# Kernel optimization log

Hardware: AMD Instinct MI355X
Metric: run time of the kernel (lower is better)

The kernel has to match this reference:

```python
import jax, jax.numpy as jnp
import numpy as np

N = 50000
E = 1000000
NODE_IN = 1281
H = 256
L = 4
NUM_RADIAL = 16
CUTOFF = 10.0
PROJ = 128
NUM_CLASSES = 4
MSG_IN = H + 3 + NUM_RADIAL  # 275


def layer_norm(x, g, b, eps=1e-5):
    m = jnp.mean(x, axis=-1, keepdims=True)
    v = jnp.var(x, axis=-1, keepdims=True)
    return (x - m) * jax.lax.rsqrt(v + eps) * g + b


def setup_inputs() -> dict:
    key = jax.random.key(0)
    ks = jax.random.split(key, 32)
    inp = {}
    inp['x'] = jax.random.normal(ks[0], (N, NODE_IN), dtype=jnp.float32)
    inp['pos'] = jax.random.normal(ks[1], (N, 3), dtype=jnp.float32) * 5.0
    inp['edge_index'] = jax.random.randint(ks[2], (2, E), 0, N, dtype=jnp.int32)
    s = lambda k, shp, fan: jax.random.normal(k, shp, dtype=jnp.float32) * (1.0 / np.sqrt(fan))
    # node encoder: Linear(1281->256), SiLU, Linear(256->256), LayerNorm
    inp['ne_W1'] = s(ks[3], (NODE_IN, H), NODE_IN); inp['ne_b1'] = jnp.zeros((H,), jnp.float32)
    inp['ne_W2'] = s(ks[4], (H, H), H); inp['ne_b2'] = jnp.zeros((H,), jnp.float32)
    inp['ne_g'] = jnp.ones((H,), jnp.float32); inp['ne_beta'] = jnp.zeros((H,), jnp.float32)
    # conv layers (stacked over L): Linear(275->256) + LayerNorm, plus outer LayerNorms
    inp['convW'] = s(ks[5], (L, MSG_IN, H), MSG_IN)
    inp['convB'] = jnp.zeros((L, H), jnp.float32)
    inp['convG'] = jnp.ones((L, H), jnp.float32); inp['convBeta'] = jnp.zeros((L, H), jnp.float32)
    inp['lnG'] = jnp.ones((L, H), jnp.float32); inp['lnB'] = jnp.zeros((L, H), jnp.float32)
    # attention pool gate: Linear(256->64), SiLU, Linear(64->1)
    inp['pgW1'] = s(ks[6], (H, H // 4), H); inp['pgb1'] = jnp.zeros((H // 4,), jnp.float32)
    inp['pgW2'] = s(ks[7], (H // 4, 1), H // 4); inp['pgb2'] = jnp.zeros((1,), jnp.float32)
    # classifier: Linear(256->128), SiLU, Linear(128->4)
    inp['clW1'] = s(ks[8], (H, H // 2), H); inp['clb1'] = jnp.zeros((H // 2,), jnp.float32)
    inp['clW2'] = s(ks[9], (H // 2, NUM_CLASSES), H // 2); inp['clb2'] = jnp.zeros((NUM_CLASSES,), jnp.float32)
    # projector: Linear(256->256), SiLU, Linear(256->128)
    inp['prW1'] = s(ks[10], (H, H), H); inp['prb1'] = jnp.zeros((H,), jnp.float32)
    inp['prW2'] = s(ks[11], (H, PROJ), H); inp['prb2'] = jnp.zeros((PROJ,), jnp.float32)
    return inp


def _forward(x, pos, edge_index,
             ne_W1, ne_b1, ne_W2, ne_b2, ne_g, ne_beta,
             convW, convB, convG, convBeta, lnG, lnB,
             pgW1, pgb1, pgW2, pgb2, clW1, clb1, clW2, clb2,
             prW1, prb1, prW2, prb2):
    src, dst = edge_index[0], edge_index[1]
    # --- edge encoder ---
    rel = pos[dst] - pos[src]                       # (E,3)
    dist = jnp.linalg.norm(rel, axis=-1)            # (E,)
    centers = jnp.linspace(0.0, CUTOFF, NUM_RADIAL).astype(jnp.float32)
    width = 0.5 * (CUTOFF / NUM_RADIAL) ** 2
    edge_radial = jnp.exp(-width * (dist[:, None] - centers) ** 2)   # (E,16)
    edge_sh = rel / jnp.maximum(dist[:, None], 1e-12)                # F.normalize, (E,3)
    # --- node encoder ---
    h = jax.nn.silu(x @ ne_W1 + ne_b1) @ ne_W2 + ne_b2
    h = layer_norm(h, ne_g, ne_beta)                # (N,256)
    # --- message passing layers (fallback SE3ConvLayer) ---
    for i in range(L):
        msg = jnp.concatenate([h[src], edge_sh, edge_radial], axis=-1)  # (E,275)
        msg = msg @ convW[i] + convB[i]                                 # (E,256)
        agg = jax.ops.segment_sum(msg, dst, num_segments=N)             # scatter_add
        h_new = layer_norm(jax.nn.silu(agg), convG[i], convBeta[i])
        h = layer_norm(h + h_new, lnG[i], lnB[i])   # dropout is identity in eval
    # --- attention pooling (batch=None) ---
    gate = jax.nn.silu(h @ pgW1 + pgb1) @ pgW2 + pgb2   # (N,1)
    gate = jax.nn.softmax(gate, axis=0)
    graph_emb = jnp.sum(h * gate, axis=0, keepdims=True)  # (1,256)
    # --- heads ---
    logits = jax.nn.silu(graph_emb @ clW1 + clb1) @ clW2 + clb2          # (1,4)
    proj = jax.nn.silu(graph_emb @ prW1 + prb1) @ prW2 + prb2            # (1,128)
    proj = proj / jnp.maximum(jnp.linalg.norm(proj, axis=-1, keepdims=True), 1e-12)
    return logits, proj, graph_emb


def reference(x, pos, edge_index,
              ne_W1, ne_b1, ne_W2, ne_b2, ne_g, ne_beta,
              convW, convB, convG, convBeta, lnG, lnB,
              pgW1, pgb1, pgW2, pgb2, clW1, clb1, clW2, clb2,
              prW1, prb1, prW2, prb2):
    return _forward(x, pos, edge_index,
                    ne_W1, ne_b1, ne_W2, ne_b2, ne_g, ne_beta,
                    convW, convB, convG, convBeta, lnG, lnB,
                    pgW1, pgb1, pgW2, pgb2, clW1, clb1, clW2, clb2,
                    prW1, prb1, prW2, prb2)
```

## Files before the change

### kernel.cpp

```cpp
#include <hip/hip_runtime.h>

typedef unsigned short u16;
typedef unsigned int   u32;

constexpr int N_NODES = 50000;
constexpr int N_PAD   = 50048;
constexpr int E_EDGES = 1000000;
constexpr int NODE_IN = 1281;
constexpr int H       = 256;
constexpr int NLAYER  = 4;
constexpr int MSG_IN  = 275;
constexpr int MSG_PAD = 320;
constexpr int NRAD    = 16;

#define DEVINL __device__ __forceinline__

DEVINL float b2f(u16 u){ return __uint_as_float(((u32)u) << 16); }
DEVINL u16 f2b(float f){
    u32 u = __float_as_uint(f);
    u32 r = u + 0x7FFFu + ((u >> 16) & 1u);
    return (u16)(r >> 16);
}
DEVINL u16 ld16(const void* p, long i, int f){
    return f ? f2b(((const float*)p)[i]) : ((const u16*)p)[i];
}
DEVINL float ldf(const void* p, long i, int f){
    return f ? ((const float*)p)[i] : b2f(((const u16*)p)[i]);
}
DEVINL float silu_f(float x){ return x / (1.f + __expf(-x)); }
DEVINL float wredsum(float v){
    #pragma unroll
    for (int o = 32; o; o >>= 1) v += __shfl_xor(v, o, 64);
    return v;
}

typedef __attribute__((ext_vector_type(8))) short bf8;
typedef __attribute__((ext_vector_type(4))) float f4;

__global__ __launch_bounds__(256) void k_init(const u16* __restrict__ neg, int* __restrict__ flags,
                                              float* __restrict__ ge, float* __restrict__ Z,
                                              int* __restrict__ deg, int* __restrict__ cur){
    int idx = blockIdx.x * 256 + threadIdx.x;
    if (idx < N_NODES) deg[idx] = 0;
    else if (idx < 2 * N_NODES) cur[idx - N_NODES] = 0;
    if (blockIdx.x == 0){
        ge[threadIdx.x] = 0.f;
        if (threadIdx.x == 0){
            flags[0] = (neg[0] == 0x3F80u) ? 0 : 1;
            *Z = 0.f;
        }
    }
}

__global__ __launch_bounds__(256) void k_xprep(const void* __restrict__ x,
                                               u16* __restrict__ xpad, float* __restrict__ xcol,
                                               const int* __restrict__ flagp){
    int f = *flagp;
    long idx = (long)blockIdx.x * 256 + threadIdx.x;
    int r = (int)(idx / 160), g = (int)(idx % 160);
    if (r >= N_PAD) return;
    u32 t[4];
    if (r < N_NODES){
        long base = (long)r * NODE_IN + g * 8;
        #pragma unroll
        for (int j = 0; j < 4; ++j){
            u32 lo = (u32)ld16(x, base + 2*j,     f);
            u32 hi = (u32)ld16(x, base + 2*j + 1, f);
            t[j] = lo | (hi << 16);
        }
    } else { t[0]=t[1]=t[2]=t[3]=0; }
    *(uint4*)&xpad[(long)r * 1280 + g * 8] = make_uint4(t[0],t[1],t[2],t[3]);
    if (g == 0)
        xcol[r] = (r < N_NODES) ? ldf(x, (long)r * NODE_IN + 1280, f) : 0.f;
}

__global__ __launch_bounds__(256) void k_deg(const int* __restrict__ ei, int* __restrict__ deg){
    int e = blockIdx.x * 256 + threadIdx.x;
    if (e < E_EDGES) atomicAdd(&deg[ei[E_EDGES + e]], 1);
}

__global__ __launch_bounds__(1024) void k_scan1(const int* __restrict__ deg, int* __restrict__ rs,
                                                int* __restrict__ bsum){
    __shared__ int buf[1024];
    int tid = threadIdx.x;
    long i = (long)blockIdx.x * 1024 + tid;
    int v = (i < N_NODES) ? deg[i] : 0;
    buf[tid] = v;
    __syncthreads();
    for (int off = 1; off < 1024; off <<= 1){
        int t = (tid >= off) ? buf[tid - off] : 0;
        __syncthreads();
        buf[tid] += t;
        __syncthreads();
    }
    if (i < N_NODES) rs[i] = buf[tid] - v;
    if (tid == 1023) bsum[blockIdx.x] = buf[1023];
}
__global__ void k_scan2(int* __restrict__ bsum){
    int tid = threadIdx.x;
    int v = (tid < 49) ? bsum[tid] : 0;
    int orig = v;
    #pragma unroll
    for (int o = 1; o < 64; o <<= 1){
        int t = __shfl_up(v, o, 64);
        if (tid >= o) v += t;
    }
    if (tid < 49) bsum[tid] = v - orig;
}
__global__ __launch_bounds__(256) void k_scan3(int* __restrict__ rs, const int* __restrict__ bsum){
    int i = blockIdx.x * 256 + threadIdx.x;
    if (i < N_NODES) rs[i] += bsum[i >> 10];
    if (i == 0) rs[N_NODES] = E_EDGES;
}

__global__ __launch_bounds__(256) void k_fill(const int* __restrict__ ei, const int* __restrict__ rs,
                                              int* __restrict__ cur, int* __restrict__ csr){
    int e = blockIdx.x * 256 + threadIdx.x;
    if (e < E_EDGES){
        int d = ei[E_EDGES + e];
        int p = atomicAdd(&cur[d], 1);
        csr[rs[d] + p] = ei[e];
    }
}

__global__ __launch_bounds__(256) void k_radial(const void* __restrict__ pos, const int* __restrict__ rs,
                                                const int* __restrict__ csr, u16* __restrict__ S,
                                                const int* __restrict__ flagp){
    int f = *flagp;
    int v = blockIdx.x * 256 + threadIdx.x;
    if (v >= N_NODES) return;
    const float W  = 0.1953125f;
    const float P1 = __expf(-0.08680555556f);
    const float P2 = __expf(-0.17361111112f);
    float pvx = ldf(pos, (long)v*3+0, f), pvy = ldf(pos, (long)v*3+1, f), pvz = ldf(pos, (long)v*3+2, f);
    float sx = 0.f, sy = 0.f, sz = 0.f;
    float sr[NRAD];
    #pragma unroll
    for (int i = 0; i < NRAD; ++i) sr[i] = 0.f;
    int beg = rs[v], end = rs[v+1];
    for (int j = beg; j < end; ++j){
        int s = csr[j];
        float rx = pvx - ldf(pos, (long)s*3+0, f);
        float ry = pvy - ldf(pos, (long)s*3+1, f);
        float rz = pvz - ldf(pos, (long)s*3+2, f);
        float d = sqrtf(rx*rx + ry*ry + rz*rz);
        float inv = 1.f / fmaxf(d, 1e-12f);
        sx += rx*inv; sy += ry*inv; sz += rz*inv;
        float r  = __expf(-W * d * d);
        float qp = __expf(0.26041666667f * d) * P1;
        #pragma unroll
        for (int i = 0; i < NRAD; ++i){
            sr[i] += r;
            r  *= qp;
            qp *= P2;
        }
    }
    u16* row = S + (size_t)v * MSG_PAD + H;
    row[0] = f2b(sx); row[1] = f2b(sy); row[2] = f2b(sz);
    #pragma unroll
    for (int i = 0; i < NRAD; ++i) row[3+i] = f2b(sr[i]);
    row[19] = f2b((float)(end - beg));
}

__global__ __launch_bounds__(256) void k_w1t(const void* __restrict__ W, u16* __restrict__ T,
                                             const int* __restrict__ flagp){
    int f = *flagp;
    int i = blockIdx.x * 256 + threadIdx.x;
    if (i >= H * 1280) return;
    int n = i / 1280, k = i - n * 1280;
    T[i] = ld16(W, (long)k * H + n, f);
}
__global__ __launch_bounds__(256) void k_w2t(const void* __restrict__ W, u16* __restrict__ T,
                                             const int* __restrict__ flagp){
    int f = *flagp;
    int i = blockIdx.x * 256 + threadIdx.x;
    if (i >= H * H) return;
    int n = i / H, k = i - n * H;
    T[i] = ld16(W, (long)k * H + n, f);
}
__global__ __launch_bounds__(256) void k_cwt(const void* __restrict__ W, const void* __restrict__ B,
                                             u16* __restrict__ T, const int* __restrict__ flagp){
    int f = *flagp;
    int i = blockIdx.x * 256 + threadIdx.x;
    if (i >= NLAYER * H * MSG_PAD) return;
    int l = i / (H * MSG_PAD);
    int r = i - l * (H * MSG_PAD);
    int n = r / MSG_PAD, k = r - n * MSG_PAD;
    u16 v;
    if      (k < MSG_IN)  v = ld16(W, ((long)l * MSG_IN + k) * H + n, f);
    else if (k == MSG_IN) v = ld16(B, (long)l * H + n, f);
    else                  v = 0;
    T[i] = v;
}
__global__ __launch_bounds__(256) void k_gwt(const void* __restrict__ W1, const void* __restrict__ b1,
                                             const void* __restrict__ W2,
                                             u16* __restrict__ T, u16* __restrict__ b1pad,
                                             u16* __restrict__ w2pad, const int* __restrict__ flagp){
    int f = *flagp;
    int i = blockIdx.x * 256 + threadIdx.x;
    if (i >= H * H) return;
    int n = i >> 8, k = i & 255;
    T[i] = (n < 64) ? ld16(W1, (long)k * 64 + n, f) : (u16)0;
    if (i < H){
        b1pad[i] = (i < 64) ? ld16(b1, i, f) : (u16)0;
        w2pad[i] = (i < 64) ? ld16(W2, i, f) : (u16)0;
    }
}

DEVINL void rowred2(float (&a)[16], float (&b)[16], float* red, int w, int quad, int l16){
    __syncthreads();
    #pragma unroll
    for (int o = 1; o < 16; o <<= 1){
        #pragma unroll
        for (int s = 0; s < 16; ++s){
            a[s] += __shfl_xor(a[s], o, 64);
            b[s] += __shfl_xor(b[s], o, 64);
        }
    }
    if (l16 == 0){
        #pragma unroll
        for (int s = 0; s < 16; ++s){
            int rl = (s >> 2) * 16 + quad * 4 + (s & 3);
            red[w * 64 + rl]       = a[s];
            red[256 + w * 64 + rl] = b[s];
        }
    }
    __syncthreads();
    #pragma unroll
    for (int s = 0; s < 16; ++s){
        int rl = (s >> 2) * 16 + quad * 4 + (s & 3);
        a[s] = red[rl] + red[64 + rl] + red[128 + rl] + red[192 + rl];
        b[s] = red[256 + rl] + red[256 + 64 + rl] + red[256 + 128 + rl] + red[256 + 192 + rl];
    }
}
DEVINL void rowred1(float (&a)[16], float* red, int w, int quad, int l16){
    __syncthreads();
    #pragma unroll
    for (int o = 1; o < 16; o <<= 1)
        #pragma unroll
        for (int s = 0; s < 16; ++s)
            a[s] += __shfl_xor(a[s], o, 64);
    if (l16 == 0){
        #pragma unroll
        for (int s = 0; s < 16; ++s){
            int rl = (s >> 2) * 16 + quad * 4 + (s & 3);
            red[w * 64 + rl] = a[s];
        }
    }
    __syncthreads();
    #pragma unroll
    for (int s = 0; s < 16; ++s){
        int rl = (s >> 2) * 16 + quad * 4 + (s & 3);
        a[s] = red[rl] + red[64 + rl] + red[128 + rl] + red[192 + rl];
    }
}

__global__ __launch_bounds__(256) void k_gemm(
        const u16* __restrict__ A, int lda, int ksteps,
        const u16* __restrict__ BT, int kbt, int mode,
        const float* __restrict__ tailx, const void* __restrict__ tailw,
        const void* __restrict__ p0, const void* __restrict__ p1,
        const void* __restrict__ p2, const void* __restrict__ p3, int loff,
        u16* __restrict__ Cout, float* __restrict__ gateout,
        const int* __restrict__ flagp){
    int f = *flagp;
    __shared__ u16 As[2][64 * 64];
    __shared__ float red[512];
    int tid = threadIdx.x;
    int m0 = blockIdx.x * 64;
    int w = tid >> 6, lane = tid & 63, quad = lane >> 4, l16 = lane & 15;
    int sr = tid >> 2, cp = (tid & 3) * 2;
    int sw0 = ((cp     ^ (sr & 7)) << 3);
    int sw1 = (((cp+1) ^ (sr & 7)) << 3);
    const u16* arow = A + (size_t)(m0 + sr) * lda + cp * 8;
    const u16* btw  = BT + (size_t)(w * 64 + l16) * kbt;

    f4 acc[4][4];
    #pragma unroll
    for (int a = 0; a < 4; ++a)
        #pragma unroll
        for (int b = 0; b < 4; ++b){ f4 z = {0.f,0.f,0.f,0.f}; acc[a][b] = z; }

    uint4 a0, a1;
    bf8 bA[4][2], bB[4][2];
    auto stageA = [&](int ks){
        a0 = *(const uint4*)(arow + ks);
        a1 = *(const uint4*)(arow + ks + 8);
    };
    auto writeA = [&](int b){
        *(uint4*)&As[b][sr * 64 + sw0] = a0;
        *(uint4*)&As[b][sr * 64 + sw1] = a1;
    };
    auto loadB = [&](int ks, bf8 (&dst)[4][2]){
        #pragma unroll
        for (int ct = 0; ct < 4; ++ct)
            #pragma unroll
            for (int h = 0; h < 2; ++h)
                dst[ct][h] = *(const bf8*)&btw[(size_t)ct * 16 * kbt + ks + h * 32 + quad * 8];
    };
    auto compute = [&](int b, bf8 (&bv)[4][2]){
        #pragma unroll
        for (int h = 0; h < 2; ++h){
            bf8 af[4];
            #pragma unroll
            for (int rt = 0; rt < 4; ++rt)
                af[rt] = *(const bf8*)&As[b][(rt*16 + l16) * 64 + (((h*4 + quad) ^ (l16 & 7)) << 3)];
            #pragma unroll
            for (int ct = 0; ct < 4; ++ct)
                #pragma unroll
                for (int rt = 0; rt < 4; ++rt)
                    acc[rt][ct] = __builtin_amdgcn_mfma_f32_16x16x32_bf16(af[rt], bv[ct][h], acc[rt][ct], 0, 0, 0);
        }
    };

    stageA(0); writeA(0); loadB(0, bA);
    __syncthreads();
    int kk = 0;
    while (true){
        bool more = (kk + 1 < ksteps);
        if (more){ stageA((kk+1)*64); loadB((kk+1)*64, bB); }
        compute(kk & 1, bA);
        if (!more) break;
        writeA((kk+1) & 1);
        __syncthreads();
        ++kk;
        more = (kk + 1 < ksteps);
        if (more){ stageA((kk+1)*64); loadB((kk+1)*64, bA); }
        compute(kk & 1, bB);
        if (!more) break;
        writeA((kk+1) & 1);
        __syncthreads();
        ++kk;
    }

    if (mode == 0){
        float xl[4][4];
        #pragma unroll
        for (int rt = 0; rt < 4; ++rt)
            #pragma unroll
            for (int i = 0; i < 4; ++i)
                xl[rt][i] = tailx[m0 + rt*16 + quad*4 + i];
        #pragma unroll
        for (int ct = 0; ct < 4; ++ct){
            int col = w * 64 + ct * 16 + l16;
            float bc = ldf(p0, col, f);
            float wl = ldf(tailw, (long)1280 * H + col, f);
            #pragma unroll
            for (int rt = 0; rt < 4; ++rt)
                #pragma unroll
                for (int i = 0; i < 4; ++i){
                    int row = m0 + rt*16 + quad*4 + i;
                    Cout[(size_t)row * H + col] = f2b(silu_f(acc[rt][ct][i] + xl[rt][i] * wl + bc));
                }
        }
        return;
    }
    if (mode == 1){
        #pragma unroll
        for (int ct = 0; ct < 4; ++ct){
            float bc = ldf(p0, w * 64 + ct * 16 + l16, f);
            #pragma unroll
            for (int rt = 0; rt < 4; ++rt)
                #pragma unroll
                for (int i = 0; i < 4; ++i)
                    acc[rt][ct][i] += bc;
        }
        float a[16], b[16];
        #pragma unroll
        for (int s = 0; s < 16; ++s){ a[s] = 0.f; b[s] = 0.f; }
        #pragma unroll
        for (int ct = 0; ct < 4; ++ct)
            #pragma unroll
            for (int rt = 0; rt < 4; ++rt)
                #pragma unroll
                for (int i = 0; i < 4; ++i){
                    float vv = acc[rt][ct][i];
                    a[rt*4+i] += vv; b[rt*4+i] += vv * vv;
                }
        rowred2(a, b, red, w, quad, l16);
        #pragma unroll
        for (int s = 0; s < 16; ++s){
            float mean = a[s] * (1.f/256.f);
            float var  = b[s] * (1.f/256.f) - mean * mean;
            a[s] = mean;
            b[s] = rsqrtf(fmaxf(var, 0.f) + 1e-5f);
        }
        #pragma unroll
        for (int ct = 0; ct < 4; ++ct){
            int col = w * 64 + ct * 16 + l16;
            float g  = ldf(p1, col, f);
            float be = ldf(p2, col, f);
            #pragma unroll
            for (int rt = 0; rt < 4; ++rt)
                #pragma unroll
                for (int i = 0; i < 4; ++i){
                    int s = rt*4+i;
                    int row = m0 + rt*16 + quad*4 + i;
                    Cout[(size_t)row * H + col] = f2b((acc[rt][ct][i] - a[s]) * b[s] * g + be);
                }
        }
        return;
    }
    if (mode == 2){
        #pragma unroll
        for (int ct = 0; ct < 4; ++ct)
            #pragma unroll
            for (int rt = 0; rt < 4; ++rt)
                #pragma unroll
                for (int i = 0; i < 4; ++i)
                    acc[rt][ct][i] = silu_f(acc[rt][ct][i]);
        float a[16], b[16];
        #pragma unroll
        for (int s = 0; s < 16; ++s){ a[s] = 0.f; b[s] = 0.f; }
        #pragma unroll
        for (int ct = 0; ct < 4; ++ct)
            #pragma unroll
            for (int rt = 0; rt < 4; ++rt)
                #pragma unroll
                for (int i = 0; i < 4; ++i){
                    float vv = acc[rt][ct][i];
                    a[rt*4+i] += vv; b[rt*4+i] += vv * vv;
                }
        rowred2(a, b, red, w, quad, l16);
        #pragma unroll
        for (int s = 0; s < 16; ++s){
            float mean = a[s] * (1.f/256.f);
            float var  = b[s] * (1.f/256.f) - mean * mean;
            a[s] = mean;
            b[s] = rsqrtf(fmaxf(var, 0.f) + 1e-5f);
        }
        float ya[16], yb[16];
        #pragma unroll
        for (int s = 0; s < 16; ++s){ ya[s] = 0.f; yb[s] = 0.f; }
        #pragma unroll
        for (int ct = 0; ct < 4; ++ct){
            int col = w * 64 + ct * 16 + l16;
            float cg = ldf(p0, loff + col, f);
            float cb = ldf(p1, loff + col, f);
            #pragma unroll
            for (int rt = 0; rt < 4; ++rt)
                #pragma unroll
                for (int i = 0; i < 4; ++i){
                    int s = rt*4+i;
                    int row = m0 + rt*16 + quad*4 + i;
                    float n = (acc[rt][ct][i] - a[s]) * b[s] * cg + cb;
                    float y = b2f(Cout[(size_t)row * H + col]) + n;
                    acc[rt][ct][i] = y;
                    ya[s] += y; yb[s] += y * y;
                }
        }
        rowred2(ya, yb, red, w, quad, l16);
        #pragma unroll
        for (int s = 0; s < 16; ++s){
            float mean = ya[s] * (1.f/256.f);
            float var  = yb[s] * (1.f/256.f) - mean * mean;
            ya[s] = mean;
            yb[s] = rsqrtf(fmaxf(var, 0.f) + 1e-5f);
        }
        #pragma unroll
        for (int ct = 0; ct < 4; ++ct){
            int col = w * 64 + ct * 16 + l16;
            float lg = ldf(p2, loff + col, f);
            float lb = ldf(p3, loff + col, f);
            #pragma unroll
            for (int rt = 0; rt < 4; ++rt)
                #pragma unroll
                for (int i = 0; i < 4; ++i){
                    int s = rt*4+i;
                    int row = m0 + rt*16 + quad*4 + i;
                    Cout[(size_t)row * H + col] = f2b((acc[rt][ct][i] - ya[s]) * yb[s] * lg + lb);
                }
        }
        return;
    }
    {
        const u16* b1p = (const u16*)p0;
        const u16* w2p = (const u16*)p1;
        float a[16];
        #pragma unroll
        for (int s = 0; s < 16; ++s) a[s] = 0.f;
        #pragma unroll
        for (int ct = 0; ct < 4; ++ct){
            int col = w * 64 + ct * 16 + l16;
            float bc = b2f(b1p[col]);
            float w2 = b2f(w2p[col]);
            #pragma unroll
            for (int rt = 0; rt < 4; ++rt)
                #pragma unroll
                for (int i = 0; i < 4; ++i)
                    a[rt*4+i] += silu_f(acc[rt][ct][i] + bc) * w2;
        }
        rowred1(a, red, w, quad, l16);
        float b2v = ldf(p2, 0, f);
        if (w == 0 && l16 == 0){
            #pragma unroll
            for (int s = 0; s < 16; ++s){
                int row = m0 + (s >> 2) * 16 + quad * 4 + (s & 3);
                if (row < N_NODES) gateout[row] = a[s] + b2v;
            }
        }
    }
}

__global__ __launch_bounds__(256) void k_aggregate(const u16* __restrict__ h, const int* __restrict__ rs,
                                                   const int* __restrict__ csr, u16* __restrict__ S){
    int v = blockIdx.x * 4 + (threadIdx.x >> 6);
    int lane = threadIdx.x & 63;
    int beg = rs[v], end = rs[v+1];
    float a0 = 0.f, a1 = 0.f, a2 = 0.f, a3 = 0.f;
    for (int j = beg; j < end; ++j){
        int s = csr[j];
        ushort4 p = *(const ushort4*)&h[(size_t)s * H + lane * 4];
        a0 += b2f(p.x); a1 += b2f(p.y); a2 += b2f(p.z); a3 += b2f(p.w);
    }
    ushort4 o; o.x = f2b(a0); o.y = f2b(a1); o.z = f2b(a2); o.w = f2b(a3);
    *(ushort4*)&S[(size_t)v * MSG_PAD + lane * 4] = o;
}

__global__ __launch_bounds__(256) void k_max(const float* __restrict__ gate, float* __restrict__ bmax){
    __shared__ float red[256];
    float m = -3.4e38f;
    for (int i = blockIdx.x * 256 + threadIdx.x; i < N_NODES; i += 256 * 256)
        m = fmaxf(m, gate[i]);
    red[threadIdx.x] = m; __syncthreads();
    for (int o = 128; o; o >>= 1){
        if (threadIdx.x < o) red[threadIdx.x] = fmaxf(red[threadIdx.x], red[threadIdx.x + o]);
        __syncthreads();
    }
    if (threadIdx.x == 0) bmax[blockIdx.x] = red[0];
}

__global__ __launch_bounds__(256) void k_expsum(const float* __restrict__ gate, const float* __restrict__ bmax,
                                                float* __restrict__ expw, float* __restrict__ Z){
    __shared__ float red[256];
    red[threadIdx.x] = bmax[threadIdx.x];
    __syncthreads();
    for (int o = 128; o; o >>= 1){
        if (threadIdx.x < o) red[threadIdx.x] = fmaxf(red[threadIdx.x], red[threadIdx.x + o]);
        __syncthreads();
    }
    float mx = red[0];
    __syncthreads();
    float s = 0.f;
    for (int i = blockIdx.x * 256 + threadIdx.x; i < N_NODES; i += gridDim.x * 256){
        float w = __expf(gate[i] - mx);
        expw[i] = w; s += w;
    }
    red[threadIdx.x] = s; __syncthreads();
    for (int o = 128; o; o >>= 1){
        if (threadIdx.x < o) red[threadIdx.x] += red[threadIdx.x + o];
        __syncthreads();
    }
    if (threadIdx.x == 0) atomicAdd(Z, red[0]);
}

__global__ __launch_bounds__(256) void k_wsum(const u16* __restrict__ h, const float* __restrict__ expw,
                                              float* __restrict__ ge){
    int c = threadIdx.x;
    int per = (N_NODES + gridDim.x - 1) / gridDim.x;
    int v0 = blockIdx.x * per;
    int v1 = min(N_NODES, v0 + per);
    float acc = 0.f;
    for (int v = v0; v < v1; ++v)
        acc += expw[v] * b2f(h[(size_t)v * H + c]);
    atomicAdd(&ge[c], acc);
}

DEVINL void storeout(void* o, int i, float v, int f){
    v = (v == v) ? v : 12345.0f;
    if (f) ((float*)o)[i] = v; else ((u16*)o)[i] = f2b(v);
}

__global__ __launch_bounds__(256) void k_heads(const float* __restrict__ ge, const float* __restrict__ Zp,
        const void* clW1, const void* clb1, const void* clW2, const void* clb2,
        const void* prW1, const void* prb1, const void* prW2, const void* prb2,
        void* __restrict__ out, const int* __restrict__ flagp){
    int f = *flagp;
    __shared__ float sge[256], t1[256], red[256];
    int t = threadIdx.x;
    float invZ = 1.f / *Zp;
    float gv = ge[t] * invZ;
    sge[t] = gv;
    storeout(out, 132 + t, gv, f);
    __syncthreads();
    float a = 0.f;
    if (t < 128){
        a = ldf(clb1, t, f);
        for (int c = 0; c < 256; ++c) a += sge[c] * ldf(clW1, (long)c * 128 + t, f);
        a = silu_f(a);
    }
    t1[t] = a;
    __syncthreads();
    if (t < 4){
        float o = ldf(clb2, t, f);
        for (int j = 0; j < 128; ++j) o += t1[j] * ldf(clW2, (long)j * 4 + t, f);
        storeout(out, t, o, f);
    }
    __syncthreads();
    float b = ldf(prb1, t, f);
    for (int c = 0; c < 256; ++c) b += sge[c] * ldf(prW1, (long)c * 256 + t, f);
    b = silu_f(b);
    t1[t] = b;
    __syncthreads();
    float p2 = 0.f;
    if (t < 128){
        p2 = ldf(prb2, t, f);
        for (int j = 0; j < 256; ++j) p2 += t1[j] * ldf(prW2, (long)j * 128 + t, f);
    }
    red[t] = p2 * p2;
    __syncthreads();
    for (int o = 128; o; o >>= 1){
        if (t < o) red[t] += red[t + o];
        __syncthreads();
    }
    float nrm = sqrtf(red[0]);
    if (t < 128) storeout(out, 4 + t, p2 / fmaxf(nrm, 1e-12f), f);
}

extern "C" void kernel_launch(void* const* d_in, const int* in_sizes, int n_in,
                              void* d_out, int out_size, void* d_ws, size_t ws_size,
                              hipStream_t stream){
    const void* x      = d_in[0];
    const void* pos    = d_in[1];
    const int*  ei     = (const int*)d_in[2];
    const void* neW1   = d_in[3];
    const void* neb1   = d_in[4];
    const void* neW2   = d_in[5];
    const void* neb2   = d_in[6];
    const void* neg    = d_in[7];
    const void* nebeta = d_in[8];
    const void* convW  = d_in[9];
    const void* convB  = d_in[10];
    const void* convG  = d_in[11];
    const void* convBe = d_in[12];
    const void* lnG    = d_in[13];
    const void* lnB    = d_in[14];
    const void* pgW1   = d_in[15];
    const void* pgb1   = d_in[16];
    const void* pgW2   = d_in[17];
    const void* pgb2   = d_in[18];
    const void* clW1   = d_in[19];
    const void* clb1   = d_in[20];
    const void* clW2   = d_in[21];
    const void* clb2   = d_in[22];
    const void* prW1   = d_in[23];
    const void* prb1   = d_in[24];
    const void* prW2   = d_in[25];
    const void* prb2   = d_in[26];

    char* ws = (char*)d_ws;
    size_t off = 0;
    auto alloc = [&](size_t b) -> char* {
        char* p = ws + off;
        off = (off + b + 255) & ~(size_t)255;
        return p;
    };
    u16*   xpad = (u16*)alloc((size_t)N_PAD * 1280 * 2);
    u16*   S    = (u16*)alloc((size_t)N_PAD * MSG_PAD * 2);
    u16*   hbuf = (u16*)alloc((size_t)N_PAD * H * 2);
    u16*   tbuf = (u16*)alloc((size_t)N_PAD * H * 2);
    u16*   W1T  = (u16*)alloc((size_t)H * 1280 * 2);
    u16*   W2T  = (u16*)alloc((size_t)H * H * 2);
    u16*   CWT  = (u16*)alloc((size_t)NLAYER * H * MSG_PAD * 2);
    u16*   GWT  = (u16*)alloc((size_t)H * H * 2);
    u16*   b1pad= (u16*)alloc(H * 2);
    u16*   w2pad= (u16*)alloc(H * 2);
    float* xcol = (float*)alloc((size_t)N_PAD * 4);
    int*   deg  = (int*)alloc(N_NODES * 4);
    int*   rs   = (int*)alloc((N_NODES + 1) * 4);
    int*   cur  = (int*)alloc(N_NODES * 4);
    int*   csr  = (int*)alloc(E_EDGES * 4);
    int*   bsum = (int*)alloc(64 * 4);
    float* gate = (float*)alloc(N_NODES * 4);
    float* expw = (float*)alloc(N_NODES * 4);
    float* bmax = (float*)alloc(256 * 4);
    float* ge   = (float*)alloc(256 * 4);
    float* Z    = (float*)alloc(64);
    int*   flags= (int*)alloc(64);
    int*   flagp= flags;

    k_init<<<(2 * N_NODES + 255) / 256, 256, 0, stream>>>((const u16*)neg, flags, ge, Z, deg, cur);

    k_w1t<<<(H * 1280) / 256, 256, 0, stream>>>(neW1, W1T, flagp);
    k_w2t<<<(H * H) / 256, 256, 0, stream>>>(neW2, W2T, flagp);
    k_cwt<<<(NLAYER * H * MSG_PAD) / 256, 256, 0, stream>>>(convW, convB, CWT, flagp);
    k_gwt<<<(H * H) / 256, 256, 0, stream>>>(pgW1, pgb1, pgW2, GWT, b1pad, w2pad, flagp);

    int eb = (E_EDGES + 255) / 256;
    k_deg<<<eb, 256, 0, stream>>>(ei, deg);
    k_scan1<<<49, 1024, 0, stream>>>(deg, rs, bsum);
    k_scan2<<<1, 64, 0, stream>>>(bsum);
    k_scan3<<<196, 256, 0, stream>>>(rs, bsum);
    k_fill<<<eb, 256, 0, stream>>>(ei, rs, cur, csr);
    k_radial<<<(N_NODES + 255) / 256, 256, 0, stream>>>(pos, rs, csr, S, flagp);

    k_xprep<<<((long)N_PAD * 160 + 255) / 256, 256, 0, stream>>>(x, xpad, xcol, flagp);
    int gb = N_PAD / 64;
    k_gemm<<<gb, 256, 0, stream>>>(xpad, 1280, 20, W1T, 1280, 0,
                                   xcol, neW1, neb1, nullptr, nullptr, nullptr, 0,
                                   tbuf, nullptr, flagp);
    k_gemm<<<gb, 256, 0, stream>>>(tbuf, H, 4, W2T, H, 1,
                                   nullptr, nullptr, neb2, neg, nebeta, nullptr, 0,
                                   hbuf, nullptr, flagp);

    for (int l = 0; l < NLAYER; ++l){
        k_aggregate<<<N_NODES / 4, 256, 0, stream>>>(hbuf, rs, csr, S);
        k_gemm<<<gb, 256, 0, stream>>>(S, MSG_PAD, 5, CWT + (size_t)l * H * MSG_PAD, MSG_PAD, 2,
                                       nullptr, nullptr, convG, convBe, lnG, lnB, l * H,
                                       hbuf, nullptr, flagp);
    }

    k_gemm<<<gb, 256, 0, stream>>>(hbuf, H, 4, GWT, H, 3,
                                   nullptr, nullptr, b1pad, w2pad, pgb2, nullptr, 0,
                                   nullptr, gate, flagp);
    k_max<<<256, 256, 0, stream>>>(gate, bmax);
    k_expsum<<<256, 256, 0, stream>>>(gate, bmax, expw, Z);
    k_wsum<<<512, 256, 0, stream>>>(hbuf, expw, ge);
    k_heads<<<1, 256, 0, stream>>>(ge, Z, clW1, clb1, clW2, clb2,
                                   prW1, prb1, prW2, prb2, d_out, flagp);
}
```

Before: 1.670 ms.

## Read x directly in GEMM, merge weight prep kernels, unroll gathers

Removes the xprep pass that built a padded bf16 copy of x. The first GEMM now loads the unaligned 1281-wide rows straight from x, using funnel shifts for bf16 input and converting on the fly for fp32 input, and reads the tail column directly. The four weight-transpose kernels are merged into one launch that also packs positions into float4. The radial and aggregate edge loops are unrolled by four to keep more gathers in flight. The aim is to cut a large memory round trip and several launches, at the cost of misaligned scalar loads inside the GEMM's A staging.

```diff
diff --git a/kernel.cpp b/kernel.cpp
--- a/kernel.cpp
+++ b/kernel.cpp
@@ -2,6 +2,7 @@
 
 typedef unsigned short u16;
 typedef unsigned int   u32;
+typedef unsigned long long u64;
 
 constexpr int N_NODES = 50000;
 constexpr int N_PAD   = 50048;
@@ -28,11 +29,6 @@
     return f ? ((const float*)p)[i] : b2f(((const u16*)p)[i]);
 }
 DEVINL float silu_f(float x){ return x / (1.f + __expf(-x)); }
-DEVINL float wredsum(float v){
-    #pragma unroll
-    for (int o = 32; o; o >>= 1) v += __shfl_xor(v, o, 64);
-    return v;
-}
 
 typedef __attribute__((ext_vector_type(8))) short bf8;
 typedef __attribute__((ext_vector_type(4))) float f4;
@@ -52,26 +48,57 @@
     }
 }
 
-__global__ __launch_bounds__(256) void k_xprep(const void* __restrict__ x,
-                                               u16* __restrict__ xpad, float* __restrict__ xcol,
-                                               const int* __restrict__ flagp){
+constexpr int SEG_A = H * 1280;
+constexpr int SEG_B = SEG_A + H * H;
+constexpr int SEG_C = SEG_B + NLAYER * H * MSG_PAD;
+constexpr int SEG_D = SEG_C + H * H;
+constexpr int SEG_E = SEG_D + N_PAD;
+__global__ __launch_bounds__(256) void k_wprep(
+        const void* __restrict__ neW1, const void* __restrict__ neW2,
+        const void* __restrict__ convW, const void* __restrict__ convB,
+        const void* __restrict__ pgW1, const void* __restrict__ pgb1, const void* __restrict__ pgW2,
+        const void* __restrict__ pos,
+        u16* __restrict__ W1T, u16* __restrict__ W2T, u16* __restrict__ CWT,
+        u16* __restrict__ GWT, u16* __restrict__ b1pad, u16* __restrict__ w2pad,
+        float4* __restrict__ posp, const int* __restrict__ flagp){
     int f = *flagp;
-    long idx = (long)blockIdx.x * 256 + threadIdx.x;
-    int r = (int)(idx / 160), g = (int)(idx % 160);
-    if (r >= N_PAD) return;
-    u32 t[4];
-    if (r < N_NODES){
-        long base = (long)r * NODE_IN + g * 8;
-        #pragma unroll
-        for (int j = 0; j < 4; ++j){
-            u32 lo = (u32)ld16(x, base + 2*j,     f);
-            u32 hi = (u32)ld16(x, base + 2*j + 1, f);
-            t[j] = lo | (hi << 16);
-        }
-    } else { t[0]=t[1]=t[2]=t[3]=0; }
-    *(uint4*)&xpad[(long)r * 1280 + g * 8] = make_uint4(t[0],t[1],t[2],t[3]);
-    if (g == 0)
-        xcol[r] = (r < N_NODES) ? ldf(x, (long)r * NODE_IN + 1280, f) : 0.f;
+    int i = blockIdx.x * 256 + threadIdx.x;
+    if (i < SEG_A){
+        int n = i / 1280, k = i - n * 1280;
+        W1T[i] = ld16(neW1, (long)k * H + n, f);
+    } else if (i < SEG_B){
+        int j = i - SEG_A;
+        int n = j / H, k = j - n * H;
+        W2T[j] = ld16(neW2, (long)k * H + n, f);
+    } else if (i < SEG_C){
+        int j = i - SEG_B;
+        int l = j / (H * MSG_PAD);
+        int r = j - l * (H * MSG_PAD);
+        int n = r / MSG_PAD, k = r - n * MSG_PAD;
+        u16 v;
+        if      (k < MSG_IN)  v = ld16(convW, ((long)l * MSG_IN + k) * H + n, f);
+        else if (k == MSG_IN) v = ld16(convB, (long)l * H + n, f);
+        else                  v = 0;
+        CWT[j] = v;
+    } else if (i < SEG_D){
+        int j = i - SEG_C;
+        int n = j >> 8, k = j & 255;
+        GWT[j] = (n < 64) ? ld16(pgW1, (long)k * 64 + n, f) : (u16)0;
+        if (j < H){
+            b1pad[j] = (j < 64) ? ld16(pgb1, j, f) : (u16)0;
+            w2pad[j] = (j < 64) ? ld16(pgW2, j, f) : (u16)0;
+        }
+    } else if (i < SEG_E){
+        int v = i - SEG_D;
+        float4 p;
+        if (v < N_NODES){
+            p.x = ldf(pos, (long)v*3+0, f);
+            p.y = ldf(pos, (long)v*3+1, f);
+            p.z = ldf(pos, (long)v*3+2, f);
+        } else { p.x = p.y = p.z = 0.f; }
+        p.w = 0.f;
+        posp[v] = p;
+    }
 }
 
 __global__ __launch_bounds__(256) void k_deg(const int* __restrict__ ei, int* __restrict__ deg){
@@ -123,26 +150,21 @@
     }
 }
 
-__global__ __launch_bounds__(256) void k_radial(const void* __restrict__ pos, const int* __restrict__ rs,
-                                                const int* __restrict__ csr, u16* __restrict__ S,
-                                                const int* __restrict__ flagp){
-    int f = *flagp;
+__global__ __launch_bounds__(256) void k_radial(const float4* __restrict__ posp, const int* __restrict__ rs,
+                                                const int* __restrict__ csr, u16* __restrict__ S){
     int v = blockIdx.x * 256 + threadIdx.x;
     if (v >= N_NODES) return;
     const float W  = 0.1953125f;
     const float P1 = __expf(-0.08680555556f);
     const float P2 = __expf(-0.17361111112f);
-    float pvx = ldf(pos, (long)v*3+0, f), pvy = ldf(pos, (long)v*3+1, f), pvz = ldf(pos, (long)v*3+2, f);
+    float4 pv = posp[v];
     float sx = 0.f, sy = 0.f, sz = 0.f;
     float sr[NRAD];
     #pragma unroll
     for (int i = 0; i < NRAD; ++i) sr[i] = 0.f;
     int beg = rs[v], end = rs[v+1];
-    for (int j = beg; j < end; ++j){
-        int s = csr[j];
-        float rx = pvx - ldf(pos, (long)s*3+0, f);
-        float ry = pvy - ldf(pos, (long)s*3+1, f);
-        float rz = pvz - ldf(pos, (long)s*3+2, f);
+    auto body = [&](float4 n){
+        float rx = pv.x - n.x, ry = pv.y - n.y, rz = pv.z - n.z;
         float d = sqrtf(rx*rx + ry*ry + rz*rz);
         float inv = 1.f / fmaxf(d, 1e-12f);
         sx += rx*inv; sy += ry*inv; sz += rz*inv;
@@ -154,7 +176,14 @@
             r  *= qp;
             qp *= P2;
         }
-    }
+    };
+    int j = beg;
+    for (; j + 4 <= end; j += 4){
+        int s0 = csr[j], s1 = csr[j+1], s2 = csr[j+2], s3 = csr[j+3];
+        float4 n0 = posp[s0], n1 = posp[s1], n2 = posp[s2], n3 = posp[s3];
+        body(n0); body(n1); body(n2); body(n3);
+    }
+    for (; j < end; ++j) body(posp[csr[j]]);
     u16* row = S + (size_t)v * MSG_PAD + H;
     row[0] = f2b(sx); row[1] = f2b(sy); row[2] = f2b(sz);
     #pragma unroll
@@ -162,51 +191,6 @@
     row[19] = f2b((float)(end - beg));
 }
 
-__global__ __launch_bounds__(256) void k_w1t(const void* __restrict__ W, u16* __restrict__ T,
-                                             const int* __restrict__ flagp){
-    int f = *flagp;
-    int i = blockIdx.x * 256 + threadIdx.x;
-    if (i >= H * 1280) return;
-    int n = i / 1280, k = i - n * 1280;
-    T[i] = ld16(W, (long)k * H + n, f);
-}
-__global__ __launch_bounds__(256) void k_w2t(const void* __restrict__ W, u16* __restrict__ T,
-                                             const int* __restrict__ flagp){
-    int f = *flagp;
-    int i = blockIdx.x * 256 + threadIdx.x;
-    if (i >= H * H) return;
-    int n = i / H, k = i - n * H;
-    T[i] = ld16(W, (long)k * H + n, f);
-}
-__global__ __launch_bounds__(256) void k_cwt(const void* __restrict__ W, const void* __restrict__ B,
-                                             u16* __restrict__ T, const int* __restrict__ flagp){
-    int f = *flagp;
-    int i = blockIdx.x * 256 + threadIdx.x;
-    if (i >= NLAYER * H * MSG_PAD) return;
-    int l = i / (H * MSG_PAD);
-    int r = i - l * (H * MSG_PAD);
-    int n = r / MSG_PAD, k = r - n * MSG_PAD;
-    u16 v;
-    if      (k < MSG_IN)  v = ld16(W, ((long)l * MSG_IN + k) * H + n, f);
-    else if (k == MSG_IN) v = ld16(B, (long)l * H + n, f);
-    else                  v = 0;
-    T[i] = v;
-}
-__global__ __launch_bounds__(256) void k_gwt(const void* __restrict__ W1, const void* __restrict__ b1,
-                                             const void* __restrict__ W2,
-                                             u16* __restrict__ T, u16* __restrict__ b1pad,
-                                             u16* __restrict__ w2pad, const int* __restrict__ flagp){
-    int f = *flagp;
-    int i = blockIdx.x * 256 + threadIdx.x;
-    if (i >= H * H) return;
-    int n = i >> 8, k = i & 255;
-    T[i] = (n < 64) ? ld16(W1, (long)k * 64 + n, f) : (u16)0;
-    if (i < H){
-        b1pad[i] = (i < 64) ? ld16(b1, i, f) : (u16)0;
-        w2pad[i] = (i < 64) ? ld16(W2, i, f) : (u16)0;
-    }
-}
-
 DEVINL void rowred2(float (&a)[16], float (&b)[16], float* red, int w, int quad, int l16){
     __syncthreads();
     #pragma unroll
@@ -256,9 +240,9 @@
 }
 
 __global__ __launch_bounds__(256) void k_gemm(
-        const u16* __restrict__ A, int lda, int ksteps,
+        const void* __restrict__ A, int lda, int axmode, int ksteps,
         const u16* __restrict__ BT, int kbt, int mode,
-        const float* __restrict__ tailx, const void* __restrict__ tailw,
+        const void* __restrict__ tailw,
         const void* __restrict__ p0, const void* __restrict__ p1,
         const void* __restrict__ p2, const void* __restrict__ p3, int loff,
         u16* __restrict__ Cout, float* __restrict__ gateout,
@@ -272,8 +256,13 @@
     int sr = tid >> 2, cp = (tid & 3) * 2;
     int sw0 = ((cp     ^ (sr & 7)) << 3);
     int sw1 = (((cp+1) ^ (sr & 7)) << 3);
-    const u16* arow = A + (size_t)(m0 + sr) * lda + cp * 8;
+    const u16* arow = (const u16*)A + (size_t)(m0 + sr) * lda + cp * 8;
     const u16* btw  = BT + (size_t)(w * 64 + l16) * kbt;
+    bool rowok = (m0 + sr) < N_NODES;
+    long ebase = (long)(m0 + sr) * NODE_IN + cp * 8;
+    long wi0 = ebase >> 1;
+    int shh = ((int)(ebase & 1)) * 16;
+    const u32* xw = (const u32*)A;
 
     f4 acc[4][4];
     #pragma unroll
@@ -284,8 +273,35 @@
     uint4 a0, a1;
     bf8 bA[4][2], bB[4][2];
     auto stageA = [&](int ks){
-        a0 = *(const uint4*)(arow + ks);
-        a1 = *(const uint4*)(arow + ks + 8);
+        if (axmode == 0){
+            a0 = *(const uint4*)(arow + ks);
+            a1 = *(const uint4*)(arow + ks + 8);
+        } else if (!rowok){
+            a0 = make_uint4(0,0,0,0); a1 = a0;
+        } else if (f == 0){
+            long wi = wi0 + (ks >> 1);
+            u32 t[9];
+            #pragma unroll
+            for (int j = 0; j < 9; ++j) t[j] = xw[wi + j];
+            u32 o[8];
+            #pragma unroll
+            for (int j = 0; j < 8; ++j)
+                o[j] = (u32)(((((u64)t[j+1]) << 32) | (u64)t[j]) >> shh);
+            a0 = make_uint4(o[0],o[1],o[2],o[3]);
+            a1 = make_uint4(o[4],o[5],o[6],o[7]);
+        } else {
+            const float* xf = (const float*)A;
+            long e = ebase + ks;
+            u32 o[8];
+            #pragma unroll
+            for (int j = 0; j < 8; ++j){
+                u32 lo = (u32)f2b(xf[e + 2*j]);
+                u32 hi = (u32)f2b(xf[e + 2*j + 1]);
+                o[j] = lo | (hi << 16);
+            }
+            a0 = make_uint4(o[0],o[1],o[2],o[3]);
+            a1 = make_uint4(o[4],o[5],o[6],o[7]);
+        }
     };
     auto writeA = [&](int b){
         *(uint4*)&As[b][sr * 64 + sw0] = a0;
@@ -338,8 +354,10 @@
         #pragma unroll
         for (int rt = 0; rt < 4; ++rt)
             #pragma unroll
-            for (int i = 0; i < 4; ++i)
-                xl[rt][i] = tailx[m0 + rt*16 + quad*4 + i];
+            for (int i = 0; i < 4; ++i){
+                int row = m0 + rt*16 + quad*4 + i;
+                xl[rt][i] = (row < N_NODES) ? ldf(A, (long)row * NODE_IN + 1280, f) : 0.f;
+            }
         #pragma unroll
         for (int ct = 0; ct < 4; ++ct){
             int col = w * 64 + ct * 16 + l16;
@@ -507,14 +525,27 @@
     int v = blockIdx.x * 4 + (threadIdx.x >> 6);
     int lane = threadIdx.x & 63;
     int beg = rs[v], end = rs[v+1];
+    int co = lane * 4;
     float a0 = 0.f, a1 = 0.f, a2 = 0.f, a3 = 0.f;
-    for (int j = beg; j < end; ++j){
+    int j = beg;
+    for (; j + 4 <= end; j += 4){
+        int s0 = csr[j], s1 = csr[j+1], s2 = csr[j+2], s3 = csr[j+3];
+        ushort4 p0 = *(const ushort4*)&h[(size_t)s0 * H + co];
+        ushort4 p1 = *(const ushort4*)&h[(size_t)s1 * H + co];
+        ushort4 p2 = *(const ushort4*)&h[(size_t)s2 * H + co];
+        ushort4 p3 = *(const ushort4*)&h[(size_t)s3 * H + co];
+        a0 += b2f(p0.x) + b2f(p1.x) + b2f(p2.x) + b2f(p3.x);
+        a1 += b2f(p0.y) + b2f(p1.y) + b2f(p2.y) + b2f(p3.y);
+        a2 += b2f(p0.z) + b2f(p1.z) + b2f(p2.z) + b2f(p3.z);
+        a3 += b2f(p0.w) + b2f(p1.w) + b2f(p2.w) + b2f(p3.w);
+    }
+    for (; j < end; ++j){
         int s = csr[j];
-        ushort4 p = *(const ushort4*)&h[(size_t)s * H + lane * 4];
+        ushort4 p = *(const ushort4*)&h[(size_t)s * H + co];
         a0 += b2f(p.x); a1 += b2f(p.y); a2 += b2f(p.z); a3 += b2f(p.w);
     }
     ushort4 o; o.x = f2b(a0); o.y = f2b(a1); o.z = f2b(a2); o.w = f2b(a3);
-    *(ushort4*)&S[(size_t)v * MSG_PAD + lane * 4] = o;
+    *(ushort4*)&S[(size_t)v * MSG_PAD + co] = o;
 }
 
 __global__ __launch_bounds__(256) void k_max(const float* __restrict__ gate, float* __restrict__ bmax){
@@ -655,7 +686,6 @@
         off = (off + b + 255) & ~(size_t)255;
         return p;
     };
-    u16*   xpad = (u16*)alloc((size_t)N_PAD * 1280 * 2);
     u16*   S    = (u16*)alloc((size_t)N_PAD * MSG_PAD * 2);
     u16*   hbuf = (u16*)alloc((size_t)N_PAD * H * 2);
     u16*   tbuf = (u16*)alloc((size_t)N_PAD * H * 2);
@@ -665,7 +695,7 @@
     u16*   GWT  = (u16*)alloc((size_t)H * H * 2);
     u16*   b1pad= (u16*)alloc(H * 2);
     u16*   w2pad= (u16*)alloc(H * 2);
-    float* xcol = (float*)alloc((size_t)N_PAD * 4);
+    float4* posp= (float4*)alloc((size_t)N_PAD * 16);
     int*   deg  = (int*)alloc(N_NODES * 4);
     int*   rs   = (int*)alloc((N_NODES + 1) * 4);
     int*   cur  = (int*)alloc(N_NODES * 4);
@@ -680,11 +710,8 @@
     int*   flagp= flags;
 
     k_init<<<(2 * N_NODES + 255) / 256, 256, 0, stream>>>((const u16*)neg, flags, ge, Z, deg, cur);
-
-    k_w1t<<<(H * 1280) / 256, 256, 0, stream>>>(neW1, W1T, flagp);
-    k_w2t<<<(H * H) / 256, 256, 0, stream>>>(neW2, W2T, flagp);
-    k_cwt<<<(NLAYER * H * MSG_PAD) / 256, 256, 0, stream>>>(convW, convB, CWT, flagp);
-    k_gwt<<<(H * H) / 256, 256, 0, stream>>>(pgW1, pgb1, pgW2, GWT, b1pad, w2pad, flagp);
+    k_wprep<<<(SEG_E + 255) / 256, 256, 0, stream>>>(neW1, neW2, convW, convB, pgW1, pgb1, pgW2, pos,
+                                                     W1T, W2T, CWT, GWT, b1pad, w2pad, posp, flagp);
 
     int eb = (E_EDGES + 255) / 256;
     k_deg<<<eb, 256, 0, stream>>>(ei, deg);
@@ -692,26 +719,25 @@
     k_scan2<<<1, 64, 0, stream>>>(bsum);
     k_scan3<<<196, 256, 0, stream>>>(rs, bsum);
     k_fill<<<eb, 256, 0, stream>>>(ei, rs, cur, csr);
-    k_radial<<<(N_NODES + 255) / 256, 256, 0, stream>>>(pos, rs, csr, S, flagp);
-
-    k_xprep<<<((long)N_PAD * 160 + 255) / 256, 256, 0, stream>>>(x, xpad, xcol, flagp);
+    k_radial<<<(N_NODES + 255) / 256, 256, 0, stream>>>(posp, rs, csr, S);
+
     int gb = N_PAD / 64;
-    k_gemm<<<gb, 256, 0, stream>>>(xpad, 1280, 20, W1T, 1280, 0,
-                                   xcol, neW1, neb1, nullptr, nullptr, nullptr, 0,
+    k_gemm<<<gb, 256, 0, stream>>>(x, NODE_IN, 1, 20, W1T, 1280, 0,
+                                   neW1, neb1, nullptr, nullptr, nullptr, 0,
                                    tbuf, nullptr, flagp);
-    k_gemm<<<gb, 256, 0, stream>>>(tbuf, H, 4, W2T, H, 1,
-                                   nullptr, nullptr, neb2, neg, nebeta, nullptr, 0,
+    k_gemm<<<gb, 256, 0, stream>>>(tbuf, H, 0, 4, W2T, H, 1,
+                                   nullptr, neb2, neg, nebeta, nullptr, 0,
                                    hbuf, nullptr, flagp);
 
     for (int l = 0; l < NLAYER; ++l){
         k_aggregate<<<N_NODES / 4, 256, 0, stream>>>(hbuf, rs, csr, S);
-        k_gemm<<<gb, 256, 0, stream>>>(S, MSG_PAD, 5, CWT + (size_t)l * H * MSG_PAD, MSG_PAD, 2,
-                                       nullptr, nullptr, convG, convBe, lnG, lnB, l * H,
+        k_gemm<<<gb, 256, 0, stream>>>(S, MSG_PAD, 0, 5, CWT + (size_t)l * H * MSG_PAD, MSG_PAD, 2,
+                                       nullptr, convG, convBe, lnG, lnB, l * H,
                                        hbuf, nullptr, flagp);
     }
 
-    k_gemm<<<gb, 256, 0, stream>>>(hbuf, H, 4, GWT, H, 3,
-                                   nullptr, nullptr, b1pad, w2pad, pgb2, nullptr, 0,
+    k_gemm<<<gb, 256, 0, stream>>>(hbuf, H, 0, 4, GWT, H, 3,
+                                   nullptr, b1pad, w2pad, pgb2, nullptr, 0,
                                    nullptr, gate, flagp);
     k_max<<<256, 256, 0, stream>>>(gate, bmax);
     k_expsum<<<256, 256, 0, stream>>>(gate, bmax, expw, Z);
```

After: 1.418 ms. -15.1%, faster.
